# Optimization experiments

Measured on AMD Instinct MI355X. Metric: run time of the kernel, lower is better.

## Reference

```python
import jax, jax.numpy as jnp
import numpy as np
from jax import lax

DIM, HEADS, HID = 192, 8, int(192 * 2.66)  # HID = 510
B, H, W = 8, 128, 128


def _ln(x, w, b):
    # WithBias LayerNorm over channel dim (to_3d puts C last, so per-pixel over C)
    mu = x.mean(1, keepdims=True)
    var = ((x - mu) ** 2).mean(1, keepdims=True)
    return (x - mu) / jnp.sqrt(var + 1e-5) * w[None, :, None, None] + b[None, :, None, None]


def _c1(x, w):  # 1x1 conv, w: [O, C]
    return jnp.einsum('bchw,oc->bohw', x, w)


def _dw(x, w):  # depthwise 3x3, w: [C, 1, 3, 3]
    return lax.conv_general_dilated(x, w, (1, 1), 'SAME',
                                    dimension_numbers=('NCHW', 'OIHW', 'NCHW'),
                                    feature_group_count=x.shape[1])


def _film(x, k_v, Wk):
    m = k_v @ Wk.T                       # [b, 2c]
    c = x.shape[1]
    return x * m[:, :c, None, None] + m[:, c:, None, None]


def _double_norm(t):
    # custom_normalize (norm + eps) followed by F.normalize (max(norm, eps)), dim=-1
    n1 = jnp.sqrt((t * t).sum(-1, keepdims=True)) + 1e-12
    t = t / n1
    n2 = jnp.sqrt((t * t).sum(-1, keepdims=True))
    return t / jnp.maximum(n2, 1e-12)


def setup_inputs() -> dict:
    key = jax.random.key(0)
    ks = jax.random.split(key, 12)
    s = 0.05
    return {
        'x': jax.random.normal(ks[0], (B, DIM, H, W), jnp.float32),
        'k_v': jax.random.normal(ks[1], (B, 256), jnp.float32),
        'ln1_w': jnp.ones((DIM,), jnp.float32),
        'ln1_b': jnp.zeros((DIM,), jnp.float32),
        'attn_kern': jax.random.normal(ks[2], (2 * DIM, 256), jnp.float32) * 0.02,
        'qkv_w': jax.random.normal(ks[3], (3 * DIM, DIM), jnp.float32) * s,
        'qkv_dw_w': jax.random.normal(ks[4], (3 * DIM, 1, 3, 3), jnp.float32) * s,
        'proj_w': jax.random.normal(ks[5], (DIM, DIM), jnp.float32) * s,
        'temperature': jnp.ones((HEADS, 1, 1), jnp.float32),
        'ln2_w': jnp.ones((DIM,), jnp.float32),
        'ln2_b': jnp.zeros((DIM,), jnp.float32),
        'ffn_kern': jax.random.normal(ks[6], (2 * DIM, 256), jnp.float32) * 0.02,
        'pin_w': jax.random.normal(ks[7], (2 * HID, DIM), jnp.float32) * s,
        'ffn_dw_w': jax.random.normal(ks[8], (2 * HID, 1, 3, 3), jnp.float32) * s,
        'pout_w': jax.random.normal(ks[9], (DIM, HID), jnp.float32) * s,
    }


def reference(x, k_v, ln1_w, ln1_b, attn_kern, qkv_w, qkv_dw_w, proj_w, temperature,
              ln2_w, ln2_b, ffn_kern, pin_w, ffn_dw_w, pout_w):
    b, c, h, w = x.shape
    cf = c // HEADS

    # ---- attention branch ----
    xn = _film(_ln(x, ln1_w, ln1_b), k_v, attn_kern)
    qkv = _dw(_c1(xn, qkv_w), qkv_dw_w)              # [b, 3c, h, w]
    q, k, v = jnp.split(qkv, 3, axis=1)
    q = _double_norm(q.reshape(b, HEADS, cf, h * w))
    k = _double_norm(k.reshape(b, HEADS, cf, h * w))
    v = v.reshape(b, HEADS, cf, h * w)
    attn = jnp.einsum('bhcn,bhdn->bhcd', q, k) * temperature  # channel attention [b,H,cf,cf]
    attn = jax.nn.softmax(attn, axis=-1)
    out = jnp.einsum('bhcd,bhdn->bhcn', attn, v).reshape(b, c, h, w)
    x = x + _c1(out, proj_w)

    # ---- gated conv FFN branch ----
    xn = _film(_ln(x, ln2_w, ln2_b), k_v, ffn_kern)
    u = _dw(_c1(xn, pin_w), ffn_dw_w)                # [b, 2*HID, h, w]
    u1, u2 = jnp.split(u, 2, axis=1)
    u = jax.nn.gelu(u1, approximate=False) * u2
    x = x + _c1(u, pout_w)
    return x  # k_v passes through unchanged
```

## Files before the change

### kernel.cpp

```cpp
#include <hip/hip_runtime.h>
#include <math.h>

#define NB 8
#define NC 192
#define NHEADS 8
#define NCF 24
#define NHW 16384
#define NWID 128
#define CQKV 576
#define OQKV_PAD 640
#define CPIN 1024
#define CG 512
#define OM_PAD 256

typedef unsigned short bfu;
typedef __bf16 bf16x8 __attribute__((ext_vector_type(8)));
typedef float f32x4 __attribute__((ext_vector_type(4)));

__device__ __forceinline__ float b2f(unsigned short u) { return __uint_as_float(((unsigned)u) << 16); }
__device__ __forceinline__ unsigned short f2b(float f) {
    unsigned u = __float_as_uint(f);
    u += 0x7FFFu + ((u >> 16) & 1u);
    return (unsigned short)(u >> 16);
}
__device__ __forceinline__ float gelu_tanh(float x) {
    float x3 = x * x * x;
    float z = 0.7978845608028654f * fmaf(0.044715f, x3, x);
    float e = __expf(2.f * z);
    float th = 1.f - 2.f / (e + 1.f);
    return 0.5f * x * (1.f + th);
}

struct F8 { float v[8]; };
__device__ __forceinline__ F8 load8(const bfu* p) {
    uint4 r = *(const uint4*)p;
    F8 o;
    o.v[0] = b2f((unsigned short)(r.x & 0xffff)); o.v[1] = b2f((unsigned short)(r.x >> 16));
    o.v[2] = b2f((unsigned short)(r.y & 0xffff)); o.v[3] = b2f((unsigned short)(r.y >> 16));
    o.v[4] = b2f((unsigned short)(r.z & 0xffff)); o.v[5] = b2f((unsigned short)(r.z >> 16));
    o.v[6] = b2f((unsigned short)(r.w & 0xffff)); o.v[7] = b2f((unsigned short)(r.w >> 16));
    return o;
}
__device__ __forceinline__ void store8(bfu* p, const float* a) {
    uint4 r;
    r.x = (unsigned)f2b(a[0]) | ((unsigned)f2b(a[1]) << 16);
    r.y = (unsigned)f2b(a[2]) | ((unsigned)f2b(a[3]) << 16);
    r.z = (unsigned)f2b(a[4]) | ((unsigned)f2b(a[5]) << 16);
    r.w = (unsigned)f2b(a[6]) | ((unsigned)f2b(a[7]) << 16);
    *(uint4*)p = r;
}

__global__ __launch_bounds__(256) void zfill(float* __restrict__ p, int n) {
    int i = blockIdx.x * 256 + threadIdx.x;
    if (i < n) p[i] = 0.f;
}

__global__ __launch_bounds__(256) void prep_film(
    const float* __restrict__ kv, const float* __restrict__ kern,
    const float* __restrict__ lnw, const float* __restrict__ lnb,
    float* __restrict__ sArr, float* __restrict__ tArr)
{
    const int b = blockIdx.y;
    const int wave = threadIdx.x >> 6, lane = threadIdx.x & 63;
    const int r = blockIdx.x * 4 + wave;
    const float* kvb = kv + b * 256;
    float4 kvv = *(const float4*)(kvb + lane * 4);
    float4 k1 = *(const float4*)(kern + (size_t)r * 256 + lane * 4);
    float4 k2 = *(const float4*)(kern + (size_t)(r + NC) * 256 + lane * 4);
    float d1 = kvv.x * k1.x + kvv.y * k1.y + kvv.z * k1.z + kvv.w * k1.w;
    float d2 = kvv.x * k2.x + kvv.y * k2.y + kvv.z * k2.z + kvv.w * k2.w;
    #pragma unroll
    for (int off = 32; off; off >>= 1) {
        d1 += __shfl_down(d1, off, 64);
        d2 += __shfl_down(d2, off, 64);
    }
    if (lane == 0) {
        sArr[b * NC + r] = lnw[r] * d1;
        tArr[b * NC + r] = lnb[r] * d1 + d2;
    }
}

__global__ __launch_bounds__(256) void wprep(
    const float* __restrict__ W, const float* __restrict__ sA, const float* __restrict__ tA,
    bfu* __restrict__ Abf, float* __restrict__ u, float* __restrict__ v0, int mode)
{
    const int wave = threadIdx.x >> 6, lane = threadIdx.x & 63;
    const int o = blockIdx.x * 4 + wave;
    const int b = blockIdx.y;
    const int Opad = (mode == 0) ? OQKV_PAD : (mode == 1 ? CPIN : OM_PAD);
    const int K = (mode == 2) ? 512 : 192;
    const int Kr = (mode == 2) ? 510 : 192;
    const int K32 = K >> 5;
    int src;
    if (mode == 0) src = (o < 576) ? o : -1;
    else if (mode == 1) src = (o < 510) ? o : (o < 512 ? -1 : (o < 1022 ? o - 2 : -1));
    else src = (o < 192) ? o : -1;
    const float* wr = (src >= 0) ? W + (size_t)src * Kr : nullptr;
    const float* sb = sA + b * NC;
    const float* tb = tA + b * NC;
    bfu* abase = Abf + (size_t)b * Opad * K;
    float au = 0.f, av = 0.f;
    for (int c0 = lane * 4; c0 < K; c0 += 256) {
        float a[4] = {0.f, 0.f, 0.f, 0.f};
        if (src >= 0) {
            #pragma unroll
            for (int j = 0; j < 4; ++j) {
                int c = c0 + j;
                if (c < Kr) {
                    float w = wr[c];
                    if (mode == 2) a[j] = w;
                    else { a[j] = w * sb[c]; av = fmaf(w, tb[c], av); }
                }
            }
        }
        ushort4 pk;
        bfu b0 = f2b(a[0]), b1 = f2b(a[1]), b2 = f2b(a[2]), b3 = f2b(a[3]);
        pk.x = b0; pk.y = b1; pk.z = b2; pk.w = b3;
        au += b2f(b0) + b2f(b1) + b2f(b2) + b2f(b3);
        int frag = (o >> 4) * K32 + (c0 >> 5);
        int within = ((c0 >> 3) & 3) * 128 + (o & 15) * 8 + (c0 & 7);
        *(ushort4*)(abase + (size_t)frag * 512 + within) = pk;
    }
    if (mode < 2) {
        #pragma unroll
        for (int off = 32; off; off >>= 1) {
            au += __shfl_down(au, off, 64);
            av += __shfl_down(av, off, 64);
        }
        if (lane == 0) {
            u[(size_t)b * Opad + o] = au;
            v0[(size_t)b * Opad + o] = (src >= 0) ? av : 0.f;
        }
    }
}

__global__ __launch_bounds__(256) void wdw_prep(
    const float* __restrict__ src, float* __restrict__ dstT, int C, int mode)
{
    int i = blockIdx.x * 256 + threadIdx.x;
    if (i >= 9 * C) return;
    int tap = i / C, col = i % C;
    float v;
    if (mode == 0) v = src[(size_t)col * 9 + tap];
    else {
        if (col < 512) v = (col < 510) ? src[(size_t)col * 9 + tap] : 0.f;
        else { int c2 = col - 512; v = (c2 < 510) ? src[(size_t)(510 + c2) * 9 + tap] : 0.f; }
    }
    dstT[(size_t)tap * C + col] = v;
}

__global__ __launch_bounds__(256) void ln_cvt_cm(
    const float* __restrict__ x, float* __restrict__ mu, float* __restrict__ rstd,
    bfu* __restrict__ xbf, int cb)
{
    __shared__ bfu lt[64][198];
    const int blkpx = blockIdx.x;
    const int b = blkpx >> 8;
    const int n0 = (blkpx & 255) * 64;
    const int tid = threadIdx.x;
    #pragma unroll
    for (int it = 0; it < 12; ++it) {
        int task = it * 256 + tid;
        int c = task >> 4, q = task & 15;
        float4 v = *(const float4*)(x + ((size_t)b * NC + c) * NHW + n0 + q * 4);
        lt[q * 4 + 0][c] = f2b(v.x);
        lt[q * 4 + 1][c] = f2b(v.y);
        lt[q * 4 + 2][c] = f2b(v.z);
        lt[q * 4 + 3][c] = f2b(v.w);
    }
    __syncthreads();
    {
        int px = tid >> 2, part = tid & 3;
        const unsigned* row = (const unsigned*)&lt[px][0];
        float s = 0.f, ss = 0.f;
        #pragma unroll
        for (int i = 0; i < 24; ++i) {
            unsigned w = row[part * 24 + i];
            float a = b2f((unsigned short)(w & 0xffff));
            float bb = b2f((unsigned short)(w >> 16));
            s += a + bb; ss = fmaf(a, a, ss); ss = fmaf(bb, bb, ss);
        }
        s += __shfl_down(s, 2, 4); ss += __shfl_down(ss, 2, 4);
        s += __shfl_down(s, 1, 4); ss += __shfl_down(ss, 1, 4);
        if (part == 0) {
            int idx = b * NHW + n0 + px;
            float m = s * (1.f / 192.f);
            float var = ss * (1.f / 192.f) - m * m;
            mu[idx] = m;
            rstd[idx] = rsqrtf(var + 1e-5f);
        }
    }
    #pragma unroll
    for (int it = 0; it < 6; ++it) {
        int task = it * 256 + tid;
        int px = task / 24, ckk = task % 24;
        const unsigned* row = (const unsigned*)&lt[px][0];
        uint4 o;
        o.x = row[ckk * 4 + 0]; o.y = row[ckk * 4 + 1];
        o.z = row[ckk * 4 + 2]; o.w = row[ckk * 4 + 3];
        *(uint4*)(xbf + ((size_t)b * NHW + n0 + px) * NC + ckk * 8) = o;
    }
}

__global__ __launch_bounds__(256) void ln_stats_pm8(
    const bfu* __restrict__ xpm, float* __restrict__ mu, float* __restrict__ rstd, int cb)
{
    int gt = blockIdx.x * 256 + threadIdx.x;
    int px = gt >> 3, seg = gt & 7;
    if (px >= cb * NHW) return;
    const bfu* row = xpm + (size_t)px * NC;
    float s = 0.f, ss = 0.f;
    #pragma unroll
    for (int it = 0; it < 3; ++it) {
        F8 v = load8(row + (seg + it * 8) * 8);
        #pragma unroll
        for (int j = 0; j < 8; ++j) { s += v.v[j]; ss = fmaf(v.v[j], v.v[j], ss); }
    }
    #pragma unroll
    for (int off = 4; off; off >>= 1) {
        s += __shfl_down(s, off, 8);
        ss += __shfl_down(ss, off, 8);
    }
    if (seg == 0) {
        float m = s * (1.f / 192.f);
        float var = ss * (1.f / 192.f) - m * m;
        mu[px] = m;
        rstd[px] = rsqrtf(var + 1e-5f);
    }
}

template<int EPI>
__global__ __launch_bounds__(256) void gemm_pm(
    const bfu* __restrict__ A, long aBStride, int Opad, int Oreal, int K,
    const bfu* __restrict__ X, int xRow, int xOff,
    void* __restrict__ Y, int yRow,
    const void* __restrict__ res, int resRow,
    const float* __restrict__ mu, const float* __restrict__ rstd,
    const float* __restrict__ uvec, const float* __restrict__ v0vec, int uStride)
{
    constexpr int SMEM = (EPI == 3) ? (64 * 129 * 4) : (2 * 64 * 72 * 2);
    __shared__ __align__(16) char smem[SMEM];
    bfu* xsbuf = (bfu*)smem;
    bfu (*stg)[136] = (bfu(*)[136])smem;
    float (*stg32)[129] = (float(*)[129])smem;

    const int b = blockIdx.z;
    const int om = blockIdx.y * 128;
    const int n0 = blockIdx.x * 64;
    const int tid = threadIdx.x;
    const int lane = tid & 63, wave = tid >> 6;
    const int wy = wave >> 1, wx = wave & 1;
    const int l15 = lane & 15, kg = lane >> 4;
    const int K32 = K >> 5;
    const int NCH = K >> 6;
    const int o16b = (om >> 4) + wy * 4;

    const bfu* Ab = A + (size_t)b * aBStride;
    const bfu* Xbase = X + ((size_t)b * NHW + n0) * xRow + xOff;
    const int sr = tid >> 3, sc = tid & 7;

    f32x4 acc[4][2];
    #pragma unroll
    for (int i = 0; i < 4; ++i)
        #pragma unroll
        for (int j = 0; j < 2; ++j) acc[i][j] = (f32x4){0.f, 0.f, 0.f, 0.f};

    #pragma unroll
    for (int i = 0; i < 2; ++i) {
        int r = i * 32 + sr;
        uint4 v = *(const uint4*)(Xbase + (size_t)r * xRow + sc * 8);
        *(uint4*)&xsbuf[(r) * 72 + sc * 8] = v;
    }
    __syncthreads();

    for (int kc = 0; kc < NCH; ++kc) {
        const int cur = kc & 1;
        if (kc + 1 < NCH) {
            #pragma unroll
            for (int i = 0; i < 2; ++i) {
                int r = i * 32 + sr;
                uint4 v = *(const uint4*)(Xbase + (size_t)r * xRow + (kc + 1) * 64 + sc * 8);
                *(uint4*)&xsbuf[((cur ^ 1) * 64 + r) * 72 + sc * 8] = v;
            }
        }
        #pragma unroll
        for (int ks = 0; ks < 2; ++ks) {
            const int k32 = kc * 2 + ks;
            bf16x8 af[4], bfr[2];
            #pragma unroll
            for (int mf = 0; mf < 4; ++mf)
                af[mf] = *(const bf16x8*)(Ab + ((size_t)(o16b + mf) * K32 + k32) * 512 + lane * 8);
            #pragma unroll
            for (int nf = 0; nf < 2; ++nf)
                bfr[nf] = *(const bf16x8*)&xsbuf[(cur * 64 + wx * 32 + nf * 16 + l15) * 72 + ks * 32 + kg * 8];
            #pragma unroll
            for (int mf = 0; mf < 4; ++mf)
                #pragma unroll
                for (int nf = 0; nf < 2; ++nf)
                    acc[mf][nf] = __builtin_amdgcn_mfma_f32_16x16x32_bf16(af[mf], bfr[nf], acc[mf][nf], 0, 0, 0);
        }
        __syncthreads();
    }

    #pragma unroll
    for (int nf = 0; nf < 2; ++nf) {
        const int nl = wx * 32 + nf * 16 + l15;
        float muv = 0.f, rsv = 0.f;
        if (EPI == 0) {
            muv = mu[(size_t)b * NHW + n0 + nl];
            rsv = rstd[(size_t)b * NHW + n0 + nl];
        }
        #pragma unroll
        for (int mf = 0; mf < 4; ++mf) {
            const int obl = wy * 64 + mf * 16 + kg * 4;
            if (EPI == 3) {
                stg32[nl][obl + 0] = acc[mf][nf][0];
                stg32[nl][obl + 1] = acc[mf][nf][1];
                stg32[nl][obl + 2] = acc[mf][nf][2];
                stg32[nl][obl + 3] = acc[mf][nf][3];
            } else {
                float r0, r1, r2, r3;
                if (EPI == 0) {
                    float4 uv = *(const float4*)(uvec + (size_t)b * uStride + om + obl);
                    float4 vv = *(const float4*)(v0vec + (size_t)b * uStride + om + obl);
                    r0 = rsv * (acc[mf][nf][0] - muv * uv.x) + vv.x;
                    r1 = rsv * (acc[mf][nf][1] - muv * uv.y) + vv.y;
                    r2 = rsv * (acc[mf][nf][2] - muv * uv.z) + vv.z;
                    r3 = rsv * (acc[mf][nf][3] - muv * uv.w) + vv.w;
                } else {
                    r0 = acc[mf][nf][0]; r1 = acc[mf][nf][1];
                    r2 = acc[mf][nf][2]; r3 = acc[mf][nf][3];
                }
                ushort4 pk;
                pk.x = f2b(r0); pk.y = f2b(r1); pk.z = f2b(r2); pk.w = f2b(r3);
                *(ushort4*)&stg[nl][obl] = pk;
            }
        }
    }
    __syncthreads();

    if (EPI == 3) {
        #pragma unroll
        for (int it = 0; it < 8; ++it) {
            int task = it * 256 + tid;
            int o = task >> 4, q = task & 15;
            int oc = om + o;
            if (oc >= Oreal) continue;
            float vals[4];
            #pragma unroll
            for (int j = 0; j < 4; ++j) {
                float v = stg32[q * 4 + j][o];
                float r = b2f(((const bfu*)res)[((size_t)b * NHW + n0 + q * 4 + j) * resRow + oc]);
                vals[j] = v + r;
            }
            *(float4*)((float*)Y + ((size_t)b * NC + oc) * NHW + n0 + q * 4) =
                make_float4(vals[0], vals[1], vals[2], vals[3]);
        }
    } else {
        #pragma unroll
        for (int it = 0; it < 4; ++it) {
            int task = it * 256 + tid;
            int nl = task >> 4, ch = task & 15;
            int oc = om + ch * 8;
            if (oc >= Oreal) continue;
            uint4 sv = *(const uint4*)&stg[nl][ch * 8];
            size_t nglob = (size_t)b * NHW + n0 + nl;
            if (EPI == 0) {
                *(uint4*)((bfu*)Y + nglob * yRow + oc) = sv;
            } else {
                float a[8];
                a[0] = b2f((unsigned short)(sv.x & 0xffff)); a[1] = b2f((unsigned short)(sv.x >> 16));
                a[2] = b2f((unsigned short)(sv.y & 0xffff)); a[3] = b2f((unsigned short)(sv.y >> 16));
                a[4] = b2f((unsigned short)(sv.z & 0xffff)); a[5] = b2f((unsigned short)(sv.z >> 16));
                a[6] = b2f((unsigned short)(sv.w & 0xffff)); a[7] = b2f((unsigned short)(sv.w >> 16));
                F8 rv = load8((const bfu*)res + nglob * resRow + oc);
                #pragma unroll
                for (int j = 0; j < 8; ++j) a[j] += rv.v[j];
                store8((bfu*)Y + nglob * yRow + oc, a);
            }
        }
    }
}

template<int CIN>
__global__ __launch_bounds__(256) void dw_pm8(
    const bfu* __restrict__ in, const float* __restrict__ wT, bfu* __restrict__ out, int cb)
{
    const int CHUNKS = CIN / 8;
    const int NPB = NHW / 8;
    int f = blockIdx.x * 256 + threadIdx.x;
    if (f >= cb * NPB * CHUNKS) return;
    int ch = f % CHUNKS;
    int pb = f / CHUNKS;
    int n8 = pb & (NPB - 1);
    int b  = pb >> 11;
    int xq = n8 & 15, y = n8 >> 4;
    int x0 = xq * 8;
    const int c8 = ch * 8;
    const bfu* rowb = in + ((size_t)b * NHW + (size_t)y * NWID) * CIN + c8;

    float acc[8][8] = {};
    #pragma unroll
    for (int dy = -1; dy <= 1; ++dy) {
        int yy = y + dy;
        if ((unsigned)yy >= (unsigned)NWID) continue;
        const bfu* rb = rowb + (long)dy * NWID * CIN;
        float w1[3][8];
        #pragma unroll
        for (int t = 0; t < 3; ++t) {
            const float* wp = wT + (size_t)((dy + 1) * 3 + t) * CIN + c8;
            *(float4*)&w1[t][0] = *(const float4*)wp;
            *(float4*)&w1[t][4] = *(const float4*)(wp + 4);
        }
        #pragma unroll
        for (int c = 0; c < 10; ++c) {
            int xx = x0 - 1 + c;
            if ((unsigned)xx >= (unsigned)NWID) continue;
            F8 v = load8(rb + (size_t)xx * CIN);
            #pragma unroll
            for (int j = 0; j < 8; ++j) {
                int t = c - j;
                if (t < 0 || t > 2) continue;
                #pragma unroll
                for (int e = 0; e < 8; ++e)
                    acc[j][e] = fmaf(w1[t][e], v.v[e], acc[j][e]);
            }
        }
    }
    #pragma unroll
    for (int j = 0; j < 8; ++j)
        store8(out + ((size_t)b * NHW + (size_t)y * NWID + x0 + j) * CIN + c8, acc[j]);
}

template<int CIN, int COUT>
__global__ __launch_bounds__(256) void dw_gate(
    const bfu* __restrict__ in, const float* __restrict__ wT, bfu* __restrict__ out, int cb)
{
    const int CHUNKS = COUT / 8;
    const int NPB = NHW / 4;
    int f = blockIdx.x * 256 + threadIdx.x;
    if (f >= cb * NPB * CHUNKS) return;
    int ch = f % CHUNKS;
    int pb = f / CHUNKS;
    int n4 = pb & (NPB - 1);
    int b  = pb >> 12;
    int xb = n4 & 31, y = n4 >> 5;
    int x0 = xb * 4;
    const int c8 = ch * 8;
    const bfu* rowb = in + ((size_t)b * NHW + (size_t)y * NWID) * CIN + c8;

    float a1[4][8] = {};
    float a2[4][8] = {};
    #pragma unroll
    for (int dy = -1; dy <= 1; ++dy) {
        int yy = y + dy;
        if ((unsigned)yy >= (unsigned)NWID) continue;
        const bfu* rb = rowb + (long)dy * NWID * CIN;
        float w1[3][8], w2[3][8];
        #pragma unroll
        for (int t = 0; t < 3; ++t) {
            const float* wp = wT + (size_t)((dy + 1) * 3 + t) * CIN + c8;
            *(float4*)&w1[t][0] = *(const float4*)wp;
            *(float4*)&w1[t][4] = *(const float4*)(wp + 4);
            *(float4*)&w2[t][0] = *(const float4*)(wp + 512);
            *(float4*)&w2[t][4] = *(const float4*)(wp + 516);
        }
        #pragma unroll
        for (int c = 0; c < 6; ++c) {
            int xx = x0 - 1 + c;
            if ((unsigned)xx >= (unsigned)NWID) continue;
            F8 v1 = load8(rb + (size_t)xx * CIN);
            F8 v2 = load8(rb + (size_t)xx * CIN + 512);
            #pragma unroll
            for (int j = 0; j < 4; ++j) {
                int t = c - j;
                if (t < 0 || t > 2) continue;
                #pragma unroll
                for (int e = 0; e < 8; ++e) {
                    a1[j][e] = fmaf(w1[t][e], v1.v[e], a1[j][e]);
                    a2[j][e] = fmaf(w2[t][e], v2.v[e], a2[j][e]);
                }
            }
        }
    }
    #pragma unroll
    for (int j = 0; j < 4; ++j) {
        float r[8];
        #pragma unroll
        for (int e = 0; e < 8; ++e) r[e] = gelu_tanh(a1[j][e]) * a2[j][e];
        store8(out + ((size_t)b * NHW + (size_t)y * NWID + x0 + j) * COUT + c8, r);
    }
}

__global__ __launch_bounds__(256) void gram_pm(
    const bfu* __restrict__ qkv, float* __restrict__ S32,
    float* __restrict__ Q2, float* __restrict__ K2, int b0)
{
    __shared__ bfu lds[392 * 72];
    const int b = blockIdx.y;
    const int nc = blockIdx.x;
    const int tid = threadIdx.x;
    const int lane = tid & 63, wave = tid >> 6;
    const int l15 = lane & 15, kg = lane >> 4;

    f32x4 sAcc[2][2][2], qAcc[2][2], kAcc[2][2];
    #pragma unroll
    for (int h = 0; h < 2; ++h)
        #pragma unroll
        for (int i = 0; i < 2; ++i) {
            qAcc[h][i] = (f32x4){0.f, 0.f, 0.f, 0.f};
            kAcc[h][i] = (f32x4){0.f, 0.f, 0.f, 0.f};
            #pragma unroll
            for (int j = 0; j < 2; ++j) sAcc[h][i][j] = (f32x4){0.f, 0.f, 0.f, 0.f};
        }

    const size_t pbase = (size_t)b * NHW + (size_t)nc * 256;
    unsigned* ldsw = (unsigned*)lds;

    for (int it = 0; it < 4; ++it) {
        const size_t nb = pbase + it * 64;
        #pragma unroll
        for (int i = 0; i < 6; ++i) {
            int task = i * 256 + tid;
            int np = task & 31, ch = task >> 5;
            const bfu* r0 = qkv + (nb + np * 2) * CQKV + ch * 8;
            uint4 v0 = *(const uint4*)r0;
            uint4 v1 = *(const uint4*)(r0 + CQKV);
            int cb8 = ch * 8;
            ldsw[(cb8 + 0) * 36 + np] = (v0.x & 0xffffu) | (v1.x << 16);
            ldsw[(cb8 + 1) * 36 + np] = (v0.x >> 16) | (v1.x & 0xffff0000u);
            ldsw[(cb8 + 2) * 36 + np] = (v0.y & 0xffffu) | (v1.y << 16);
            ldsw[(cb8 + 3) * 36 + np] = (v0.y >> 16) | (v1.y & 0xffff0000u);
            ldsw[(cb8 + 4) * 36 + np] = (v0.z & 0xffffu) | (v1.z << 16);
            ldsw[(cb8 + 5) * 36 + np] = (v0.z >> 16) | (v1.z & 0xffff0000u);
            ldsw[(cb8 + 6) * 36 + np] = (v0.w & 0xffffu) | (v1.w << 16);
            ldsw[(cb8 + 7) * 36 + np] = (v0.w >> 16) | (v1.w & 0xffff0000u);
        }
        ldsw[(384 + (tid >> 5)) * 36 + (tid & 31)] = 0;
        __syncthreads();
        #pragma unroll
        for (int hh = 0; hh < 2; ++hh) {
            const int h = wave * 2 + hh;
            const int qr = h * NCF, kr = NC + h * NCF;
            #pragma unroll
            for (int ks = 0; ks < 2; ++ks) {
                const int nsub = ks * 32 + kg * 8;
                bf16x8 aq0 = *(const bf16x8*)(lds + (qr + l15) * 72 + nsub);
                bf16x8 aq1 = *(const bf16x8*)(lds + (qr + 16 + l15) * 72 + nsub);
                bf16x8 bk0 = *(const bf16x8*)(lds + (kr + l15) * 72 + nsub);
                bf16x8 bk1 = *(const bf16x8*)(lds + (kr + 16 + l15) * 72 + nsub);
                sAcc[hh][0][0] = __builtin_amdgcn_mfma_f32_16x16x32_bf16(aq0, bk0, sAcc[hh][0][0], 0, 0, 0);
                sAcc[hh][0][1] = __builtin_amdgcn_mfma_f32_16x16x32_bf16(aq0, bk1, sAcc[hh][0][1], 0, 0, 0);
                sAcc[hh][1][0] = __builtin_amdgcn_mfma_f32_16x16x32_bf16(aq1, bk0, sAcc[hh][1][0], 0, 0, 0);
                sAcc[hh][1][1] = __builtin_amdgcn_mfma_f32_16x16x32_bf16(aq1, bk1, sAcc[hh][1][1], 0, 0, 0);
                qAcc[hh][0] = __builtin_amdgcn_mfma_f32_16x16x32_bf16(aq0, aq0, qAcc[hh][0], 0, 0, 0);
                qAcc[hh][1] = __builtin_amdgcn_mfma_f32_16x16x32_bf16(aq1, aq1, qAcc[hh][1], 0, 0, 0);
                kAcc[hh][0] = __builtin_amdgcn_mfma_f32_16x16x32_bf16(bk0, bk0, kAcc[hh][0], 0, 0, 0);
                kAcc[hh][1] = __builtin_amdgcn_mfma_f32_16x16x32_bf16(bk1, bk1, kAcc[hh][1], 0, 0, 0);
            }
        }
        __syncthreads();
    }

    const int gb = b0 + b;
    #pragma unroll
    for (int hh = 0; hh < 2; ++hh) {
        const int h = wave * 2 + hh;
        float* Sp = S32 + ((size_t)gb * NHEADS + h) * 1024;
        #pragma unroll
        for (int mt = 0; mt < 2; ++mt)
            #pragma unroll
            for (int nt = 0; nt < 2; ++nt)
                #pragma unroll
                for (int r = 0; r < 4; ++r) {
                    int c = mt * 16 + kg * 4 + r, d = nt * 16 + l15;
                    atomicAdd(&Sp[c * 32 + d], sAcc[hh][mt][nt][r]);
                }
        #pragma unroll
        for (int t = 0; t < 2; ++t)
            #pragma unroll
            for (int r = 0; r < 4; ++r) {
                int row = t * 16 + kg * 4 + r, col = t * 16 + l15;
                if (row == col && row < NCF) {
                    atomicAdd(&Q2[((size_t)gb * NHEADS + h) * NCF + row], qAcc[hh][t][r]);
                    atomicAdd(&K2[((size_t)gb * NHEADS + h) * NCF + row], kAcc[hh][t][r]);
                }
            }
    }
}

__global__ __launch_bounds__(256) void attn_fold(
    const float* __restrict__ S32, const float* __restrict__ Q2, const float* __restrict__ K2,
    const float* __restrict__ temp, const float* __restrict__ projw, bfu* __restrict__ Mbf, int b0)
{
    const int gb = b0 + blockIdx.x, tid = threadIdx.x;
    __shared__ float P[NHEADS * NCF * NCF];
    for (int e = tid; e < NHEADS * NCF * NCF; e += 256) {
        int h = e / (NCF * NCF);
        int r = e % (NCF * NCF);
        int c = r / NCF, d = r % NCF;
        float sv = S32[((size_t)gb * NHEADS + h) * 1024 + c * 32 + d];
        float rq = sqrtf(Q2[((size_t)gb * NHEADS + h) * NCF + c]);
        float rk = sqrtf(K2[((size_t)gb * NHEADS + h) * NCF + d]);
        P[e] = sv / (rq * rk) * temp[h];
    }
    __syncthreads();
    if (tid < NHEADS * NCF) {
        int h = tid / NCF, c = tid % NCF;
        float* row = P + h * (NCF * NCF) + c * NCF;
        float mx = row[0];
        #pragma unroll
        for (int d = 1; d < NCF; ++d) mx = fmaxf(mx, row[d]);
        float sum = 0.f;
        #pragma unroll
        for (int d = 0; d < NCF; ++d) { float e2 = __expf(row[d] - mx); row[d] = e2; sum += e2; }
        float inv = 1.f / sum;
        #pragma unroll
        for (int d = 0; d < NCF; ++d) row[d] *= inv;
    }
    __syncthreads();
    bfu* Mb = Mbf + (size_t)gb * OM_PAD * NC;
    if (tid < NC) {
        int o = tid;
        int o16 = o >> 4, l15o = o & 15;
        for (int h = 0; h < NHEADS; ++h) {
            float pw[NCF];
            #pragma unroll
            for (int c = 0; c < NCF; ++c) pw[c] = projw[(size_t)o * NC + h * NCF + c];
            #pragma unroll
            for (int d = 0; d < NCF; ++d) {
                float acc = 0.f;
                #pragma unroll
                for (int c = 0; c < NCF; ++c) acc = fmaf(pw[c], P[h * (NCF * NCF) + c * NCF + d], acc);
                int cc = h * NCF + d;
                int idx = (o16 * 6 + (cc >> 5)) * 512 + ((cc >> 3) & 3) * 128 + l15o * 8 + (cc & 7);
                Mb[idx] = f2b(acc);
            }
        }
    }
    for (int e = tid; e < (OM_PAD - NC) * NC; e += 256) Mb[NC * NC + e] = 0;
}

extern "C" void kernel_launch(void* const* d_in, const int* in_sizes, int n_in,
                              void* d_out, int out_size, void* d_ws, size_t ws_size,
                              hipStream_t stream)
{
    const float* x     = (const float*)d_in[0];
    const float* kv    = (const float*)d_in[1];
    const float* ln1w  = (const float*)d_in[2];
    const float* ln1b  = (const float*)d_in[3];
    const float* akern = (const float*)d_in[4];
    const float* qkvw  = (const float*)d_in[5];
    const float* qkvdw = (const float*)d_in[6];
    const float* projw = (const float*)d_in[7];
    const float* temp  = (const float*)d_in[8];
    const float* ln2w  = (const float*)d_in[9];
    const float* ln2b  = (const float*)d_in[10];
    const float* fkern = (const float*)d_in[11];
    const float* pinw  = (const float*)d_in[12];
    const float* ffndw = (const float*)d_in[13];
    const float* poutw = (const float*)d_in[14];
    float* out = (float*)d_out;

    char* wp = (char*)d_ws;
    size_t off = 0;
    auto take = [&](size_t bytes) {
        char* r = wp + off;
        off = (off + bytes + 255) & ~(size_t)255;
        return r;
    };
    float* mu1   = (float*)take((size_t)NB * NHW * 4);
    float* rstd1 = (float*)take((size_t)NB * NHW * 4);
    float* mu2   = (float*)take((size_t)NB * NHW * 4);
    float* rstd2 = (float*)take((size_t)NB * NHW * 4);
    float* s1 = (float*)take(NB * NC * 4);  float* t1 = (float*)take(NB * NC * 4);
    float* s2 = (float*)take(NB * NC * 4);  float* t2 = (float*)take(NB * NC * 4);
    bfu* A1 = (bfu*)take((size_t)NB * OQKV_PAD * 192 * 2);
    bfu* A2 = (bfu*)take((size_t)NB * CPIN * 192 * 2);
    bfu* A3 = (bfu*)take((size_t)OM_PAD * 512 * 2);
    bfu* Mbf = (bfu*)take((size_t)NB * OM_PAD * NC * 2);
    float* u1  = (float*)take((size_t)NB * OQKV_PAD * 4);
    float* v01 = (float*)take((size_t)NB * OQKV_PAD * 4);
    float* u2  = (float*)take((size_t)NB * CPIN * 4);
    float* v02 = (float*)take((size_t)NB * CPIN * 4);
    float* wdwT1 = (float*)take(9 * CQKV * 4);
    float* wdwT2 = (float*)take(9 * CPIN * 4);
    float* S32 = (float*)take((size_t)NB * NHEADS * 1024 * 4);
    float* Q2  = (float*)take((size_t)NB * NHEADS * NCF * 4);
    float* K2  = (float*)take((size_t)NB * NHEADS * NCF * 4);
    const size_t bigoff = off;

    const size_t PB = (size_t)NHW * (384 + 384 + 2048 + 1152);
    size_t avail = (ws_size > bigoff) ? ws_size - bigoff : 0;
    int CB = 8;
    while (CB > 1 && (size_t)CB * PB > avail) CB >>= 1;

    dim3 blk(256);

    prep_film<<<dim3(48, NB), blk, 0, stream>>>(kv, akern, ln1w, ln1b, s1, t1);
    prep_film<<<dim3(48, NB), blk, 0, stream>>>(kv, fkern, ln2w, ln2b, s2, t2);
    wprep<<<dim3(OQKV_PAD / 4, NB), blk, 0, stream>>>(qkvw, s1, t1, A1, u1, v01, 0);
    wprep<<<dim3(CPIN / 4, NB), blk, 0, stream>>>(pinw, s2, t2, A2, u2, v02, 1);
    wprep<<<dim3(OM_PAD / 4, 1), blk, 0, stream>>>(poutw, s1, t1, A3, nullptr, nullptr, 2);
    wdw_prep<<<(9 * CQKV + 255) / 256, blk, 0, stream>>>(qkvdw, wdwT1, CQKV, 0);
    wdw_prep<<<(9 * CPIN + 255) / 256, blk, 0, stream>>>(ffndw, wdwT2, CPIN, 1);
    {
        int nz = NB * NHEADS * 1024 + 2 * NB * NHEADS * NCF + 256;
        zfill<<<(nz + 255) / 256, blk, 0, stream>>>(S32, nz);
    }

    for (int b0 = 0; b0 < NB; b0 += CB) {
        bfu* bfX  = (bfu*)(wp + bigoff);
        bfu* out1 = (bfu*)(wp + bigoff + (size_t)CB * NHW * 384);
        char* big1 = wp + bigoff + (size_t)CB * NHW * 768;
        char* big2 = big1 + (size_t)CB * NHW * 2048;
        bfu* qkv_pre = (bfu*)big1;
        bfu* qkvb    = (bfu*)big2;
        bfu* u_pre   = (bfu*)big1;
        bfu* gbuf    = (bfu*)big2;

        const float* xb = x + (size_t)b0 * NC * NHW;
        float* mu1b = mu1 + (size_t)b0 * NHW;   float* rs1b = rstd1 + (size_t)b0 * NHW;
        float* mu2b = mu2 + (size_t)b0 * NHW;   float* rs2b = rstd2 + (size_t)b0 * NHW;

        ln_cvt_cm<<<CB * 256, blk, 0, stream>>>(xb, mu1b, rs1b, bfX, CB);
        gemm_pm<0><<<dim3(256, OQKV_PAD / 128, CB), blk, 0, stream>>>(
            A1 + (size_t)b0 * OQKV_PAD * 192, (long)OQKV_PAD * 192, OQKV_PAD, CQKV, 192,
            bfX, NC, 0, qkv_pre, CQKV, nullptr, 0,
            mu1b, rs1b, u1 + (size_t)b0 * OQKV_PAD, v01 + (size_t)b0 * OQKV_PAD, OQKV_PAD);
        dw_pm8<CQKV><<<CB * 576, blk, 0, stream>>>(qkv_pre, wdwT1, qkvb, CB);
        gram_pm<<<dim3(64, CB), blk, 0, stream>>>(qkvb, S32, Q2, K2, b0);
        attn_fold<<<CB, blk, 0, stream>>>(S32, Q2, K2, temp, projw, Mbf, b0);
        gemm_pm<1><<<dim3(256, OM_PAD / 128, CB), blk, 0, stream>>>(
            Mbf + (size_t)b0 * OM_PAD * NC, (long)OM_PAD * NC, OM_PAD, NC, 192,
            qkvb, CQKV, 384, out1, NC, bfX, NC,
            nullptr, nullptr, nullptr, nullptr, 0);

        ln_stats_pm8<<<CB * 512, blk, 0, stream>>>(out1, mu2b, rs2b, CB);
        gemm_pm<0><<<dim3(256, CPIN / 128, CB), blk, 0, stream>>>(
            A2 + (size_t)b0 * CPIN * 192, (long)CPIN * 192, CPIN, CPIN, 192,
            out1, NC, 0, u_pre, CPIN, nullptr, 0,
            mu2b, rs2b, u2 + (size_t)b0 * CPIN, v02 + (size_t)b0 * CPIN, CPIN);
        dw_gate<CPIN, CG><<<CB * (NHW / 4) * (CG / 8) / 256, blk, 0, stream>>>(
            u_pre, wdwT2, gbuf, CB);
        gemm_pm<3><<<dim3(256, OM_PAD / 128, CB), blk, 0, stream>>>(
            A3, 0, OM_PAD, NC, 512,
            gbuf, CG, 0, out + (size_t)b0 * NC * NHW, 0, out1, NC,
            nullptr, nullptr, nullptr, nullptr, 0);
    }
}
```

Measured before the change: 836.1 us.

## Switch bf16 pipeline to fp16 with packed-half depthwise convs and full-K GEMM staging

Replaces bf16 storage and bf16 MFMA with fp16 everywhere. The depthwise and gated depthwise convolutions now accumulate in packed half2 arithmetic with fp16 weights instead of fp32 FMAs. The K=192 GEMMs stage the whole K extent in shared memory in one pass instead of double-buffering 64-wide chunks. The aim is to cut ALU cost in the depthwise kernels and remove loop and sync overhead in the GEMMs. The trade is reduced dynamic range and fp16 accumulation error in the 9-tap convolutions, plus possible overflow in fp16 activations.

```diff
diff --git a/kernel.cpp b/kernel.cpp
--- a/kernel.cpp
+++ b/kernel.cpp
@@ -14,14 +14,16 @@
 #define OM_PAD 256
 
 typedef unsigned short bfu;
-typedef __bf16 bf16x8 __attribute__((ext_vector_type(8)));
+typedef _Float16 f16x8 __attribute__((ext_vector_type(8)));
+typedef _Float16 f16x2 __attribute__((ext_vector_type(2)));
 typedef float f32x4 __attribute__((ext_vector_type(4)));
 
-__device__ __forceinline__ float b2f(unsigned short u) { return __uint_as_float(((unsigned)u) << 16); }
-__device__ __forceinline__ unsigned short f2b(float f) {
-    unsigned u = __float_as_uint(f);
-    u += 0x7FFFu + ((u >> 16) & 1u);
-    return (unsigned short)(u >> 16);
+__device__ __forceinline__ unsigned short f2h(float f) {
+    _Float16 h = (_Float16)f;
+    return __builtin_bit_cast(unsigned short, h);
+}
+__device__ __forceinline__ float h2f(unsigned short u) {
+    return (float)__builtin_bit_cast(_Float16, u);
 }
 __device__ __forceinline__ float gelu_tanh(float x) {
     float x3 = x * x * x;
@@ -32,22 +34,26 @@
 }
 
 struct F8 { float v[8]; };
-__device__ __forceinline__ F8 load8(const bfu* p) {
+union H8 { uint4 u; f16x2 h[4]; };
+__device__ __forceinline__ F8 loadh8(const bfu* p) {
     uint4 r = *(const uint4*)p;
     F8 o;
-    o.v[0] = b2f((unsigned short)(r.x & 0xffff)); o.v[1] = b2f((unsigned short)(r.x >> 16));
-    o.v[2] = b2f((unsigned short)(r.y & 0xffff)); o.v[3] = b2f((unsigned short)(r.y >> 16));
-    o.v[4] = b2f((unsigned short)(r.z & 0xffff)); o.v[5] = b2f((unsigned short)(r.z >> 16));
-    o.v[6] = b2f((unsigned short)(r.w & 0xffff)); o.v[7] = b2f((unsigned short)(r.w >> 16));
+    o.v[0] = h2f((unsigned short)(r.x & 0xffff)); o.v[1] = h2f((unsigned short)(r.x >> 16));
+    o.v[2] = h2f((unsigned short)(r.y & 0xffff)); o.v[3] = h2f((unsigned short)(r.y >> 16));
+    o.v[4] = h2f((unsigned short)(r.z & 0xffff)); o.v[5] = h2f((unsigned short)(r.z >> 16));
+    o.v[6] = h2f((unsigned short)(r.w & 0xffff)); o.v[7] = h2f((unsigned short)(r.w >> 16));
     return o;
 }
-__device__ __forceinline__ void store8(bfu* p, const float* a) {
+__device__ __forceinline__ void storeh8(bfu* p, const float* a) {
     uint4 r;
-    r.x = (unsigned)f2b(a[0]) | ((unsigned)f2b(a[1]) << 16);
-    r.y = (unsigned)f2b(a[2]) | ((unsigned)f2b(a[3]) << 16);
-    r.z = (unsigned)f2b(a[4]) | ((unsigned)f2b(a[5]) << 16);
-    r.w = (unsigned)f2b(a[6]) | ((unsigned)f2b(a[7]) << 16);
+    r.x = (unsigned)f2h(a[0]) | ((unsigned)f2h(a[1]) << 16);
+    r.y = (unsigned)f2h(a[2]) | ((unsigned)f2h(a[3]) << 16);
+    r.z = (unsigned)f2h(a[4]) | ((unsigned)f2h(a[5]) << 16);
+    r.w = (unsigned)f2h(a[6]) | ((unsigned)f2h(a[7]) << 16);
     *(uint4*)p = r;
+}
+__device__ __forceinline__ f16x2 h2z() {
+    f16x2 z; z[0] = (_Float16)0.f; z[1] = (_Float16)0.f; return z;
 }
 
 __global__ __launch_bounds__(256) void zfill(float* __restrict__ p, int n) {
@@ -114,9 +120,9 @@
             }
         }
         ushort4 pk;
-        bfu b0 = f2b(a[0]), b1 = f2b(a[1]), b2 = f2b(a[2]), b3 = f2b(a[3]);
+        bfu b0 = f2h(a[0]), b1 = f2h(a[1]), b2 = f2h(a[2]), b3 = f2h(a[3]);
         pk.x = b0; pk.y = b1; pk.z = b2; pk.w = b3;
-        au += b2f(b0) + b2f(b1) + b2f(b2) + b2f(b3);
+        au += h2f(b0) + h2f(b1) + h2f(b2) + h2f(b3);
         int frag = (o >> 4) * K32 + (c0 >> 5);
         int within = ((c0 >> 3) & 3) * 128 + (o & 15) * 8 + (c0 & 7);
         *(ushort4*)(abase + (size_t)frag * 512 + within) = pk;
@@ -135,7 +141,7 @@
 }
 
 __global__ __launch_bounds__(256) void wdw_prep(
-    const float* __restrict__ src, float* __restrict__ dstT, int C, int mode)
+    const float* __restrict__ src, bfu* __restrict__ dstT, int C, int mode)
 {
     int i = blockIdx.x * 256 + threadIdx.x;
     if (i >= 9 * C) return;
@@ -146,7 +152,7 @@
         if (col < 512) v = (col < 510) ? src[(size_t)col * 9 + tap] : 0.f;
         else { int c2 = col - 512; v = (c2 < 510) ? src[(size_t)(510 + c2) * 9 + tap] : 0.f; }
     }
-    dstT[(size_t)tap * C + col] = v;
+    dstT[(size_t)tap * C + col] = f2h(v);
 }
 
 __global__ __launch_bounds__(256) void ln_cvt_cm(
@@ -163,10 +169,10 @@
         int task = it * 256 + tid;
         int c = task >> 4, q = task & 15;
         float4 v = *(const float4*)(x + ((size_t)b * NC + c) * NHW + n0 + q * 4);
-        lt[q * 4 + 0][c] = f2b(v.x);
-        lt[q * 4 + 1][c] = f2b(v.y);
-        lt[q * 4 + 2][c] = f2b(v.z);
-        lt[q * 4 + 3][c] = f2b(v.w);
+        lt[q * 4 + 0][c] = f2h(v.x);
+        lt[q * 4 + 1][c] = f2h(v.y);
+        lt[q * 4 + 2][c] = f2h(v.z);
+        lt[q * 4 + 3][c] = f2h(v.w);
     }
     __syncthreads();
     {
@@ -176,8 +182,8 @@
         #pragma unroll
         for (int i = 0; i < 24; ++i) {
             unsigned w = row[part * 24 + i];
-            float a = b2f((unsigned short)(w & 0xffff));
-            float bb = b2f((unsigned short)(w >> 16));
+            float a = h2f((unsigned short)(w & 0xffff));
+            float bb = h2f((unsigned short)(w >> 16));
             s += a + bb; ss = fmaf(a, a, ss); ss = fmaf(bb, bb, ss);
         }
         s += __shfl_down(s, 2, 4); ss += __shfl_down(ss, 2, 4);
@@ -212,7 +218,7 @@
     float s = 0.f, ss = 0.f;
     #pragma unroll
     for (int it = 0; it < 3; ++it) {
-        F8 v = load8(row + (seg + it * 8) * 8);
+        F8 v = loadh8(row + (seg + it * 8) * 8);
         #pragma unroll
         for (int j = 0; j < 8; ++j) { s += v.v[j]; ss = fmaf(v.v[j], v.v[j], ss); }
     }
@@ -238,9 +244,10 @@
     const float* __restrict__ mu, const float* __restrict__ rstd,
     const float* __restrict__ uvec, const float* __restrict__ v0vec, int uStride)
 {
-    constexpr int SMEM = (EPI == 3) ? (64 * 129 * 4) : (2 * 64 * 72 * 2);
-    __shared__ __align__(16) char smem[SMEM];
-    bfu* xsbuf = (bfu*)smem;
+    constexpr bool FULLK = (EPI != 3);
+    constexpr int SMEMSZ = FULLK ? (64 * 208 * 2) : 33024;
+    __shared__ __align__(16) char smem[SMEMSZ];
+    bfu* xs = (bfu*)smem;
     bfu (*stg)[136] = (bfu(*)[136])smem;
     float (*stg32)[129] = (float(*)[129])smem;
 
@@ -252,12 +259,10 @@
     const int wy = wave >> 1, wx = wave & 1;
     const int l15 = lane & 15, kg = lane >> 4;
     const int K32 = K >> 5;
-    const int NCH = K >> 6;
     const int o16b = (om >> 4) + wy * 4;
 
     const bfu* Ab = A + (size_t)b * aBStride;
     const bfu* Xbase = X + ((size_t)b * NHW + n0) * xRow + xOff;
-    const int sr = tid >> 3, sc = tid & 7;
 
     f32x4 acc[4][2];
     #pragma unroll
@@ -265,41 +270,69 @@
         #pragma unroll
         for (int j = 0; j < 2; ++j) acc[i][j] = (f32x4){0.f, 0.f, 0.f, 0.f};
 
-    #pragma unroll
-    for (int i = 0; i < 2; ++i) {
-        int r = i * 32 + sr;
-        uint4 v = *(const uint4*)(Xbase + (size_t)r * xRow + sc * 8);
-        *(uint4*)&xsbuf[(r) * 72 + sc * 8] = v;
-    }
-    __syncthreads();
-
-    for (int kc = 0; kc < NCH; ++kc) {
-        const int cur = kc & 1;
-        if (kc + 1 < NCH) {
-            #pragma unroll
-            for (int i = 0; i < 2; ++i) {
-                int r = i * 32 + sr;
-                uint4 v = *(const uint4*)(Xbase + (size_t)r * xRow + (kc + 1) * 64 + sc * 8);
-                *(uint4*)&xsbuf[((cur ^ 1) * 64 + r) * 72 + sc * 8] = v;
-            }
-        }
-        #pragma unroll
-        for (int ks = 0; ks < 2; ++ks) {
-            const int k32 = kc * 2 + ks;
-            bf16x8 af[4], bfr[2];
+    if constexpr (FULLK) {
+        #pragma unroll
+        for (int i = 0; i < 6; ++i) {
+            int task = i * 256 + tid;
+            int r = task / 24, c = task % 24;
+            uint4 v = *(const uint4*)(Xbase + (size_t)r * xRow + c * 8);
+            *(uint4*)&xs[r * 208 + c * 8] = v;
+        }
+        __syncthreads();
+        #pragma unroll
+        for (int k32 = 0; k32 < 6; ++k32) {
+            f16x8 af[4], bfr[2];
             #pragma unroll
             for (int mf = 0; mf < 4; ++mf)
-                af[mf] = *(const bf16x8*)(Ab + ((size_t)(o16b + mf) * K32 + k32) * 512 + lane * 8);
+                af[mf] = *(const f16x8*)(Ab + ((size_t)(o16b + mf) * 6 + k32) * 512 + lane * 8);
             #pragma unroll
             for (int nf = 0; nf < 2; ++nf)
-                bfr[nf] = *(const bf16x8*)&xsbuf[(cur * 64 + wx * 32 + nf * 16 + l15) * 72 + ks * 32 + kg * 8];
+                bfr[nf] = *(const f16x8*)&xs[(wx * 32 + nf * 16 + l15) * 208 + k32 * 32 + kg * 8];
             #pragma unroll
             for (int mf = 0; mf < 4; ++mf)
                 #pragma unroll
                 for (int nf = 0; nf < 2; ++nf)
-                    acc[mf][nf] = __builtin_amdgcn_mfma_f32_16x16x32_bf16(af[mf], bfr[nf], acc[mf][nf], 0, 0, 0);
+                    acc[mf][nf] = __builtin_amdgcn_mfma_f32_16x16x32_f16(af[mf], bfr[nf], acc[mf][nf], 0, 0, 0);
         }
         __syncthreads();
+    } else {
+        const int sr = tid >> 3, sc = tid & 7;
+        const int NCH = K >> 6;
+        #pragma unroll
+        for (int i = 0; i < 2; ++i) {
+            int r = i * 32 + sr;
+            uint4 v = *(const uint4*)(Xbase + (size_t)r * xRow + sc * 8);
+            *(uint4*)&xs[r * 72 + sc * 8] = v;
+        }
+        __syncthreads();
+        for (int kc = 0; kc < NCH; ++kc) {
+            const int cur = kc & 1;
+            if (kc + 1 < NCH) {
+                #pragma unroll
+                for (int i = 0; i < 2; ++i) {
+                    int r = i * 32 + sr;
+                    uint4 v = *(const uint4*)(Xbase + (size_t)r * xRow + (kc + 1) * 64 + sc * 8);
+                    *(uint4*)&xs[((cur ^ 1) * 64 + r) * 72 + sc * 8] = v;
+                }
+            }
+            #pragma unroll
+            for (int ks = 0; ks < 2; ++ks) {
+                const int k32 = kc * 2 + ks;
+                f16x8 af[4], bfr[2];
+                #pragma unroll
+                for (int mf = 0; mf < 4; ++mf)
+                    af[mf] = *(const f16x8*)(Ab + ((size_t)(o16b + mf) * K32 + k32) * 512 + lane * 8);
+                #pragma unroll
+                for (int nf = 0; nf < 2; ++nf)
+                    bfr[nf] = *(const f16x8*)&xs[(cur * 64 + wx * 32 + nf * 16 + l15) * 72 + ks * 32 + kg * 8];
+                #pragma unroll
+                for (int mf = 0; mf < 4; ++mf)
+                    #pragma unroll
+                    for (int nf = 0; nf < 2; ++nf)
+                        acc[mf][nf] = __builtin_amdgcn_mfma_f32_16x16x32_f16(af[mf], bfr[nf], acc[mf][nf], 0, 0, 0);
+            }
+            __syncthreads();
+        }
     }
 
     #pragma unroll
@@ -332,7 +365,7 @@
                     r2 = acc[mf][nf][2]; r3 = acc[mf][nf][3];
                 }
                 ushort4 pk;
-                pk.x = f2b(r0); pk.y = f2b(r1); pk.z = f2b(r2); pk.w = f2b(r3);
+                pk.x = f2h(r0); pk.y = f2h(r1); pk.z = f2h(r2); pk.w = f2h(r3);
                 *(ushort4*)&stg[nl][obl] = pk;
             }
         }
@@ -350,7 +383,7 @@
             #pragma unroll
             for (int j = 0; j < 4; ++j) {
                 float v = stg32[q * 4 + j][o];
-                float r = b2f(((const bfu*)res)[((size_t)b * NHW + n0 + q * 4 + j) * resRow + oc]);
+                float r = h2f(((const bfu*)res)[((size_t)b * NHW + n0 + q * 4 + j) * resRow + oc]);
                 vals[j] = v + r;
             }
             *(float4*)((float*)Y + ((size_t)b * NC + oc) * NHW + n0 + q * 4) =
@@ -369,14 +402,14 @@
                 *(uint4*)((bfu*)Y + nglob * yRow + oc) = sv;
             } else {
                 float a[8];
-                a[0] = b2f((unsigned short)(sv.x & 0xffff)); a[1] = b2f((unsigned short)(sv.x >> 16));
-                a[2] = b2f((unsigned short)(sv.y & 0xffff)); a[3] = b2f((unsigned short)(sv.y >> 16));
-                a[4] = b2f((unsigned short)(sv.z & 0xffff)); a[5] = b2f((unsigned short)(sv.z >> 16));
-                a[6] = b2f((unsigned short)(sv.w & 0xffff)); a[7] = b2f((unsigned short)(sv.w >> 16));
-                F8 rv = load8((const bfu*)res + nglob * resRow + oc);
+                a[0] = h2f((unsigned short)(sv.x & 0xffff)); a[1] = h2f((unsigned short)(sv.x >> 16));
+                a[2] = h2f((unsigned short)(sv.y & 0xffff)); a[3] = h2f((unsigned short)(sv.y >> 16));
+                a[4] = h2f((unsigned short)(sv.z & 0xffff)); a[5] = h2f((unsigned short)(sv.z >> 16));
+                a[6] = h2f((unsigned short)(sv.w & 0xffff)); a[7] = h2f((unsigned short)(sv.w >> 16));
+                F8 rv = loadh8((const bfu*)res + nglob * resRow + oc);
                 #pragma unroll
                 for (int j = 0; j < 8; ++j) a[j] += rv.v[j];
-                store8((bfu*)Y + nglob * yRow + oc, a);
+                storeh8((bfu*)Y + nglob * yRow + oc, a);
             }
         }
     }
@@ -384,7 +417,7 @@
 
 template<int CIN>
 __global__ __launch_bounds__(256) void dw_pm8(
-    const bfu* __restrict__ in, const float* __restrict__ wT, bfu* __restrict__ out, int cb)
+    const bfu* __restrict__ in, const bfu* __restrict__ wT, bfu* __restrict__ out, int cb)
 {
     const int CHUNKS = CIN / 8;
     const int NPB = NHW / 8;
@@ -399,42 +432,51 @@
     const int c8 = ch * 8;
     const bfu* rowb = in + ((size_t)b * NHW + (size_t)y * NWID) * CIN + c8;
 
-    float acc[8][8] = {};
+    f16x2 acc[8][4];
+    #pragma unroll
+    for (int j = 0; j < 8; ++j)
+        #pragma unroll
+        for (int q = 0; q < 4; ++q) acc[j][q] = h2z();
+
     #pragma unroll
     for (int dy = -1; dy <= 1; ++dy) {
         int yy = y + dy;
         if ((unsigned)yy >= (unsigned)NWID) continue;
         const bfu* rb = rowb + (long)dy * NWID * CIN;
-        float w1[3][8];
+        f16x2 w1[3][4];
         #pragma unroll
         for (int t = 0; t < 3; ++t) {
-            const float* wp = wT + (size_t)((dy + 1) * 3 + t) * CIN + c8;
-            *(float4*)&w1[t][0] = *(const float4*)wp;
-            *(float4*)&w1[t][4] = *(const float4*)(wp + 4);
+            H8 wv; wv.u = *(const uint4*)(wT + (size_t)((dy + 1) * 3 + t) * CIN + c8);
+            #pragma unroll
+            for (int q = 0; q < 4; ++q) w1[t][q] = wv.h[q];
         }
         #pragma unroll
         for (int c = 0; c < 10; ++c) {
             int xx = x0 - 1 + c;
             if ((unsigned)xx >= (unsigned)NWID) continue;
-            F8 v = load8(rb + (size_t)xx * CIN);
+            H8 v; v.u = *(const uint4*)(rb + (size_t)xx * CIN);
             #pragma unroll
             for (int j = 0; j < 8; ++j) {
                 int t = c - j;
                 if (t < 0 || t > 2) continue;
                 #pragma unroll
-                for (int e = 0; e < 8; ++e)
-                    acc[j][e] = fmaf(w1[t][e], v.v[e], acc[j][e]);
-            }
-        }
-    }
-    #pragma unroll
-    for (int j = 0; j < 8; ++j)
-        store8(out + ((size_t)b * NHW + (size_t)y * NWID + x0 + j) * CIN + c8, acc[j]);
+                for (int q = 0; q < 4; ++q)
+                    acc[j][q] = w1[t][q] * v.h[q] + acc[j][q];
+            }
+        }
+    }
+    #pragma unroll
+    for (int j = 0; j < 8; ++j) {
+        H8 o;
+        #pragma unroll
+        for (int q = 0; q < 4; ++q) o.h[q] = acc[j][q];
+        *(uint4*)(out + ((size_t)b * NHW + (size_t)y * NWID + x0 + j) * CIN + c8) = o.u;
+    }
 }
 
 template<int CIN, int COUT>
 __global__ __launch_bounds__(256) void dw_gate(
-    const bfu* __restrict__ in, const float* __restrict__ wT, bfu* __restrict__ out, int cb)
+    const bfu* __restrict__ in, const bfu* __restrict__ wT, bfu* __restrict__ out, int cb)
 {
     const int CHUNKS = COUT / 8;
     const int NPB = NHW / 4;
@@ -449,46 +491,55 @@
     const int c8 = ch * 8;
     const bfu* rowb = in + ((size_t)b * NHW + (size_t)y * NWID) * CIN + c8;
 
-    float a1[4][8] = {};
-    float a2[4][8] = {};
+    f16x2 a1[4][4], a2[4][4];
+    #pragma unroll
+    for (int j = 0; j < 4; ++j)
+        #pragma unroll
+        for (int q = 0; q < 4; ++q) { a1[j][q] = h2z(); a2[j][q] = h2z(); }
+
     #pragma unroll
     for (int dy = -1; dy <= 1; ++dy) {
         int yy = y + dy;
         if ((unsigned)yy >= (unsigned)NWID) continue;
         const bfu* rb = rowb + (long)dy * NWID * CIN;
-        float w1[3][8], w2[3][8];
+        f16x2 w1[3][4], w2[3][4];
         #pragma unroll
         for (int t = 0; t < 3; ++t) {
-            const float* wp = wT + (size_t)((dy + 1) * 3 + t) * CIN + c8;
-            *(float4*)&w1[t][0] = *(const float4*)wp;
-            *(float4*)&w1[t][4] = *(const float4*)(wp + 4);
-            *(float4*)&w2[t][0] = *(const float4*)(wp + 512);
-            *(float4*)&w2[t][4] = *(const float4*)(wp + 516);
+            const bfu* wp = wT + (size_t)((dy + 1) * 3 + t) * CIN + c8;
+            H8 wa; wa.u = *(const uint4*)wp;
+            H8 wb; wb.u = *(const uint4*)(wp + 512);
+            #pragma unroll
+            for (int q = 0; q < 4; ++q) { w1[t][q] = wa.h[q]; w2[t][q] = wb.h[q]; }
         }
         #pragma unroll
         for (int c = 0; c < 6; ++c) {
             int xx = x0 - 1 + c;
             if ((unsigned)xx >= (unsigned)NWID) continue;
-            F8 v1 = load8(rb + (size_t)xx * CIN);
-            F8 v2 = load8(rb + (size_t)xx * CIN + 512);
+            H8 v1; v1.u = *(const uint4*)(rb + (size_t)xx * CIN);
+            H8 v2; v2.u = *(const uint4*)(rb + (size_t)xx * CIN + 512);
             #pragma unroll
             for (int j = 0; j < 4; ++j) {
                 int t = c - j;
                 if (t < 0 || t > 2) continue;
                 #pragma unroll
-                for (int e = 0; e < 8; ++e) {
-                    a1[j][e] = fmaf(w1[t][e], v1.v[e], a1[j][e]);
-                    a2[j][e] = fmaf(w2[t][e], v2.v[e], a2[j][e]);
+                for (int q = 0; q < 4; ++q) {
+                    a1[j][q] = w1[t][q] * v1.h[q] + a1[j][q];
+                    a2[j][q] = w2[t][q] * v2.h[q] + a2[j][q];
                 }
             }
         }
     }
     #pragma unroll
     for (int j = 0; j < 4; ++j) {
-        float r[8];
-        #pragma unroll
-        for (int e = 0; e < 8; ++e) r[e] = gelu_tanh(a1[j][e]) * a2[j][e];
-        store8(out + ((size_t)b * NHW + (size_t)y * NWID + x0 + j) * COUT + c8, r);
+        H8 o;
+        #pragma unroll
+        for (int q = 0; q < 4; ++q) {
+            float g0 = gelu_tanh((float)a1[j][q][0]) * (float)a2[j][q][0];
+            float g1 = gelu_tanh((float)a1[j][q][1]) * (float)a2[j][q][1];
+            f16x2 r; r[0] = (_Float16)g0; r[1] = (_Float16)g1;
+            o.h[q] = r;
+        }
+        *(uint4*)(out + ((size_t)b * NHW + (size_t)y * NWID + x0 + j) * COUT + c8) = o.u;
     }
 }
 
@@ -545,18 +596,18 @@
             #pragma unroll
             for (int ks = 0; ks < 2; ++ks) {
                 const int nsub = ks * 32 + kg * 8;
-                bf16x8 aq0 = *(const bf16x8*)(lds + (qr + l15) * 72 + nsub);
-                bf16x8 aq1 = *(const bf16x8*)(lds + (qr + 16 + l15) * 72 + nsub);
-                bf16x8 bk0 = *(const bf16x8*)(lds + (kr + l15) * 72 + nsub);
-                bf16x8 bk1 = *(const bf16x8*)(lds + (kr + 16 + l15) * 72 + nsub);
-                sAcc[hh][0][0] = __builtin_amdgcn_mfma_f32_16x16x32_bf16(aq0, bk0, sAcc[hh][0][0], 0, 0, 0);
-                sAcc[hh][0][1] = __builtin_amdgcn_mfma_f32_16x16x32_bf16(aq0, bk1, sAcc[hh][0][1], 0, 0, 0);
-                sAcc[hh][1][0] = __builtin_amdgcn_mfma_f32_16x16x32_bf16(aq1, bk0, sAcc[hh][1][0], 0, 0, 0);
-                sAcc[hh][1][1] = __builtin_amdgcn_mfma_f32_16x16x32_bf16(aq1, bk1, sAcc[hh][1][1], 0, 0, 0);
-                qAcc[hh][0] = __builtin_amdgcn_mfma_f32_16x16x32_bf16(aq0, aq0, qAcc[hh][0], 0, 0, 0);
-                qAcc[hh][1] = __builtin_amdgcn_mfma_f32_16x16x32_bf16(aq1, aq1, qAcc[hh][1], 0, 0, 0);
-                kAcc[hh][0] = __builtin_amdgcn_mfma_f32_16x16x32_bf16(bk0, bk0, kAcc[hh][0], 0, 0, 0);
-                kAcc[hh][1] = __builtin_amdgcn_mfma_f32_16x16x32_bf16(bk1, bk1, kAcc[hh][1], 0, 0, 0);
+                f16x8 aq0 = *(const f16x8*)(lds + (qr + l15) * 72 + nsub);
+                f16x8 aq1 = *(const f16x8*)(lds + (qr + 16 + l15) * 72 + nsub);
+                f16x8 bk0 = *(const f16x8*)(lds + (kr + l15) * 72 + nsub);
+                f16x8 bk1 = *(const f16x8*)(lds + (kr + 16 + l15) * 72 + nsub);
+                sAcc[hh][0][0] = __builtin_amdgcn_mfma_f32_16x16x32_f16(aq0, bk0, sAcc[hh][0][0], 0, 0, 0);
+                sAcc[hh][0][1] = __builtin_amdgcn_mfma_f32_16x16x32_f16(aq0, bk1, sAcc[hh][0][1], 0, 0, 0);
+                sAcc[hh][1][0] = __builtin_amdgcn_mfma_f32_16x16x32_f16(aq1, bk0, sAcc[hh][1][0], 0, 0, 0);
+                sAcc[hh][1][1] = __builtin_amdgcn_mfma_f32_16x16x32_f16(aq1, bk1, sAcc[hh][1][1], 0, 0, 0);
+                qAcc[hh][0] = __builtin_amdgcn_mfma_f32_16x16x32_f16(aq0, aq0, qAcc[hh][0], 0, 0, 0);
+                qAcc[hh][1] = __builtin_amdgcn_mfma_f32_16x16x32_f16(aq1, aq1, qAcc[hh][1], 0, 0, 0);
+                kAcc[hh][0] = __builtin_amdgcn_mfma_f32_16x16x32_f16(bk0, bk0, kAcc[hh][0], 0, 0, 0);
+                kAcc[hh][1] = __builtin_amdgcn_mfma_f32_16x16x32_f16(bk1, bk1, kAcc[hh][1], 0, 0, 0);
             }
         }
         __syncthreads();
@@ -634,7 +685,7 @@
                 for (int c = 0; c < NCF; ++c) acc = fmaf(pw[c], P[h * (NCF * NCF) + c * NCF + d], acc);
                 int cc = h * NCF + d;
                 int idx = (o16 * 6 + (cc >> 5)) * 512 + ((cc >> 3) & 3) * 128 + l15o * 8 + (cc & 7);
-                Mb[idx] = f2b(acc);
+                Mb[idx] = f2h(acc);
             }
         }
     }
@@ -683,8 +734,8 @@
     float* v01 = (float*)take((size_t)NB * OQKV_PAD * 4);
     float* u2  = (float*)take((size_t)NB * CPIN * 4);
     float* v02 = (float*)take((size_t)NB * CPIN * 4);
-    float* wdwT1 = (float*)take(9 * CQKV * 4);
-    float* wdwT2 = (float*)take(9 * CPIN * 4);
+    bfu* wdwT1 = (bfu*)take(9 * CQKV * 2);
+    bfu* wdwT2 = (bfu*)take(9 * CPIN * 2);
     float* S32 = (float*)take((size_t)NB * NHEADS * 1024 * 4);
     float* Q2  = (float*)take((size_t)NB * NHEADS * NCF * 4);
     float* K2  = (float*)take((size_t)NB * NHEADS * NCF * 4);
```

Result: faster. 800.9 us (-4.2%).
